# Kernel tuning notes

Measured on AMD Instinct MI355X. Metric: run time of the kernel, lower is better.

## Reference

```python
import jax, jax.numpy as jnp
import numpy as np

N_QUBITS = 6
DIM = 2 ** N_QUBITS  # 64
Q_LAYERS = 2
CHUNK = 16

# ---- single-qubit rotation gate matrices (batched over leading dim) ----

def _rx(t):
    c = jnp.cos(t / 2).astype(jnp.complex64)
    s = jnp.sin(t / 2).astype(jnp.complex64)
    return jnp.stack([jnp.stack([c, -1j * s], -1), jnp.stack([-1j * s, c], -1)], -2)

def _ry(t):
    c = jnp.cos(t / 2).astype(jnp.complex64)
    s = jnp.sin(t / 2).astype(jnp.complex64)
    return jnp.stack([jnp.stack([c, -s], -1), jnp.stack([s, c], -1)], -2)

def _rz(t):
    e = jnp.exp(-0.5j * t.astype(jnp.complex64))
    z = jnp.zeros_like(e)
    return jnp.stack([jnp.stack([e, z], -1), jnp.stack([z, jnp.conj(e)], -1)], -2)


def _apply_1q(state, gate, wire):
    # state: (B, 64) complex64; gate: (B,2,2). PennyLane wire 0 = most-significant bit.
    dl, dr = 2 ** wire, 2 ** (N_QUBITS - 1 - wire)
    s = state.reshape(-1, dl, 2, dr)
    s = jnp.einsum('bkj,bljr->blkr', gate, s)
    return s.reshape(-1, DIM)


def _apply_crx(state, theta, control, target):
    s = state.reshape((-1,) + (2,) * N_QUBITS)
    s = jnp.moveaxis(s, (control + 1, target + 1), (1, 2))
    g = _rx(theta)  # (B,2,2)
    s1 = jnp.einsum('bkj,bj...->bk...', g, s[:, 1])
    s = jnp.concatenate([s[:, :1], s1[:, None]], axis=1)
    s = jnp.moveaxis(s, (1, 2), (control + 1, target + 1))
    return s.reshape(-1, DIM)


def _ansatz(state, params, n_layers):
    # unified ansatz: per layer, RX/RY/RZ on each qubit, ring of CRX forward, ring of CRX backward
    idx = 0
    for _ in range(n_layers):
        for i in range(N_QUBITS):
            state = _apply_1q(state, _rx(params[:, idx]), i)
            state = _apply_1q(state, _ry(params[:, idx + 1]), i)
            state = _apply_1q(state, _rz(params[:, idx + 2]), i)
            idx += 3
        for i in range(N_QUBITS):
            state = _apply_crx(state, params[:, idx], i, (i + 1) % N_QUBITS)
            idx += 1
        for i in range(N_QUBITS - 1, -1, -1):
            state = _apply_crx(state, params[:, idx], i, (i - 1) % N_QUBITS)
            idx += 1
    return state


_PX = jnp.array([[0, 1], [1, 0]], jnp.complex64)
_PY = jnp.array([[0, -1j], [1j, 0]], jnp.complex64)
_PZ = jnp.array([[1, 0], [0, -1]], jnp.complex64)


def _expvals(state):
    # expectations of X_i, Y_i, Z_i for all qubits -> (B, 3*n_qubits)
    outs = []
    B = state.shape[0]
    for P in (_PX, _PY, _PZ):
        g = jnp.broadcast_to(P, (B, 2, 2))
        for i in range(N_QUBITS):
            ps = _apply_1q(state, g, i)
            outs.append(jnp.sum(jnp.conj(state) * ps, axis=1).real)
    return jnp.stack(outs, axis=1).astype(jnp.float32)


def _forward(x, emb_w, emb_b, att_w1, att_b1, att_w2, att_b2, proj_w, proj_b,
             mix_re, mix_im, qff_params, out_w, out_b, ln_g, ln_b,
             cls_w1, cls_b1, cls_w2, cls_b2):
    B, C, T = x.shape
    # classical feature extractor: (B,C,T) -> (B,T,D)
    feats = jnp.einsum('bct,cd->btd', x, emb_w) + emb_b
    D = feats.shape[-1]
    n_chunks = T // CHUNK
    xc = feats.reshape(B, n_chunks, CHUNK, D)
    # attention-weighted chunk aggregation
    h = jnp.tanh(xc @ att_w1 + att_b1)
    scores = h @ att_w2 + att_b2                      # (B,nc,CHUNK,1)
    w = jax.nn.softmax(scores, axis=2)
    chunks = jnp.sum(w * xc, axis=2)                  # (B,nc,D)
    # quantum attention core: per-chunk ansatz params
    params = jax.nn.sigmoid(chunks @ proj_w + proj_b)  # (B,nc,60)
    flat = params.reshape(B * n_chunks, -1)
    state0 = jnp.zeros((B * n_chunks, DIM), jnp.complex64).at[:, 0].set(1.0)
    evolved = _ansatz(state0, flat, Q_LAYERS).reshape(B, n_chunks, DIM)
    # LCU mixing
    coeffs = (mix_re + 1j * mix_im).astype(jnp.complex64)
    coeffs = coeffs / (jnp.abs(coeffs).sum() + 1e-8)
    mixed = jnp.einsum('bti,t->bi', evolved, coeffs)
    norms = jnp.linalg.norm(mixed, axis=1, keepdims=True)
    mixed = mixed / (norms + 1e-9)
    # quantum feed-forward (shared params) + multi-observable measurement
    qp = jnp.broadcast_to(qff_params, (B, qff_params.shape[0]))
    qstate = _ansatz(mixed, qp, 1)
    qfeat = _expvals(qstate)                          # (B,18)
    out = qfeat @ out_w + out_b                       # (B,D)
    # LayerNorm
    mu = out.mean(-1, keepdims=True)
    var = out.var(-1, keepdims=True)
    out = (out - mu) / jnp.sqrt(var + 1e-5) * ln_g + ln_b
    # classifier head
    h2 = jax.nn.relu(out @ cls_w1 + cls_b1)
    return h2 @ cls_w2 + cls_b2


def setup_inputs() -> dict:
    key = jax.random.key(0)
    ks = jax.random.split(key, 20)
    B, C, T, D = 128, 64, 2048, 256
    NC = T // CHUNK        # 128 chunks
    NCP = 5 * N_QUBITS * Q_LAYERS  # 60 circuit params
    def nrm(k, shape, scale=0.05):
        return jax.random.normal(k, shape, jnp.float32) * scale
    return {
        'x': jax.random.normal(ks[0], (B, C, T), jnp.float32),
        'emb_w': nrm(ks[1], (C, D)), 'emb_b': nrm(ks[2], (D,)),
        'att_w1': nrm(ks[3], (D, D // 2)), 'att_b1': nrm(ks[4], (D // 2,)),
        'att_w2': nrm(ks[5], (D // 2, 1)), 'att_b2': nrm(ks[6], (1,)),
        'proj_w': nrm(ks[7], (D, NCP)), 'proj_b': nrm(ks[8], (NCP,)),
        'mix_re': jax.random.uniform(ks[9], (NC,), jnp.float32),
        'mix_im': jax.random.uniform(ks[10], (NC,), jnp.float32),
        'qff_params': nrm(ks[11], (5 * N_QUBITS,), 0.1),
        'out_w': nrm(ks[12], (3 * N_QUBITS, D)), 'out_b': nrm(ks[13], (D,)),
        'ln_g': jnp.ones((D,), jnp.float32), 'ln_b': jnp.zeros((D,), jnp.float32),
        'cls_w1': nrm(ks[14], (D, D)), 'cls_b1': nrm(ks[15], (D,)),
        'cls_w2': nrm(ks[16], (D, 2)), 'cls_b2': nrm(ks[17], (2,)),
    }


def reference(x, emb_w, emb_b, att_w1, att_b1, att_w2, att_b2, proj_w, proj_b,
              mix_re, mix_im, qff_params, out_w, out_b, ln_g, ln_b,
              cls_w1, cls_b1, cls_w2, cls_b2):
    return _forward(x, emb_w, emb_b, att_w1, att_b1, att_w2, att_b2, proj_w, proj_b,
                    mix_re, mix_im, qff_params, out_w, out_b, ln_g, ln_b,
                    cls_w1, cls_b1, cls_w2, cls_b2)
```

## Files before the change

### kernel.cpp

```cpp
#include <hip/hip_runtime.h>
#include <math.h>

#define NQ    6
#define QDIM  64
#define BB    128
#define CC    64
#define TT    2048
#define DD    256
#define NCH   128
#define CHLEN 16
#define HH    128
#define NCP   60

typedef __bf16 bf16x8 __attribute__((ext_vector_type(8)));
typedef float  f32x4  __attribute__((ext_vector_type(4)));

__device__ __forceinline__ float fast_tanh(float x) {
  float e = __expf(2.f * x);
  return 1.f - 2.f / (e + 1.f);
}

__device__ __forceinline__ float wave_sum(float v) {
#pragma unroll
  for (int off = 32; off >= 1; off >>= 1) v += __shfl_xor(v, off, 64);
  return v;
}

__device__ __forceinline__ void g_rx(float& re, float& im, int lane, int m, float half) {
  float c = __cosf(half), s = __sinf(half);
  float pre = __shfl_xor(re, m, 64);
  float pim = __shfl_xor(im, m, 64);
  float nre = c * re + s * pim;
  float nim = c * im - s * pre;
  re = nre; im = nim;
}
__device__ __forceinline__ void g_ry(float& re, float& im, int lane, int m, float half) {
  float c = __cosf(half), s = __sinf(half);
  float pre = __shfl_xor(re, m, 64);
  float pim = __shfl_xor(im, m, 64);
  float sg = (lane & m) ? s : -s;
  re = c * re + sg * pre;
  im = c * im + sg * pim;
}
__device__ __forceinline__ void g_rz(float& re, float& im, int lane, int m, float half) {
  float c = __cosf(half), s = __sinf(half);
  float sg = (lane & m) ? s : -s;
  float nre = c * re - sg * im;
  float nim = c * im + sg * re;
  re = nre; im = nim;
}
__device__ __forceinline__ void g_crx(float& re, float& im, int lane, int mc, int mt, float half) {
  float c = __cosf(half), s = __sinf(half);
  float pre = __shfl_xor(re, mt, 64);
  float pim = __shfl_xor(im, mt, 64);
  if (lane & mc) {
    float nre = c * re + s * pim;
    float nim = c * im - s * pre;
    re = nre; im = nim;
  }
}
__device__ __forceinline__ void ansatz_layer(float& re, float& im, int lane,
                                             const float* p) {
#pragma unroll
  for (int q = 0; q < 6; ++q) {
    int m = 1 << (5 - q);
    g_rx(re, im, lane, m, 0.5f * p[3 * q + 0]);
    g_ry(re, im, lane, m, 0.5f * p[3 * q + 1]);
    g_rz(re, im, lane, m, 0.5f * p[3 * q + 2]);
  }
#pragma unroll
  for (int q = 0; q < 6; ++q)
    g_crx(re, im, lane, 1 << (5 - q), 1 << (5 - ((q + 1) % 6)), 0.5f * p[18 + q]);
#pragma unroll
  for (int q = 5; q >= 0; --q)
    g_crx(re, im, lane, 1 << (5 - q), 1 << (5 - ((q + 5) % 6)), 0.5f * p[24 + (5 - q)]);
}

__global__ __launch_bounds__(256) void k0_prep(
    const float* __restrict__ emb_w, const float* __restrict__ emb_b,
    const float* __restrict__ att_w1, const float* __restrict__ att_b1,
    const float* __restrict__ proj_w, const float* __restrict__ proj_b,
    __bf16* __restrict__ WfH, __bf16* __restrict__ WfL,
    __bf16* __restrict__ PfH, __bf16* __restrict__ PfL,
    float* __restrict__ b_fused, float* __restrict__ pb_fused) {
  int idx = blockIdx.x * 256 + threadIdx.x;
  if (idx < 8192) {
    int j = idx & 127, k = idx >> 7;
    float a = 0.f;
    for (int d = 0; d < 256; ++d)
      a = fmaf(emb_w[k * 256 + d], att_w1[d * 128 + j], a);
    __bf16 h = (__bf16)a;
    WfH[j * 64 + k] = h; WfL[j * 64 + k] = (__bf16)(a - (float)h);
  } else if (idx < 12288) {
    int i = idx - 8192;
    int n = i & 63, k = i >> 6;
    float a = 0.f;
    if (n < 60)
      for (int d = 0; d < 256; ++d)
        a = fmaf(emb_w[k * 256 + d], proj_w[d * 60 + n], a);
    __bf16 h = (__bf16)a;
    PfH[n * 64 + k] = h; PfL[n * 64 + k] = (__bf16)(a - (float)h);
  } else if (idx < 12416) {
    int j = idx - 12288;
    float a = att_b1[j];
    for (int d = 0; d < 256; ++d) a = fmaf(emb_b[d], att_w1[d * 128 + j], a);
    b_fused[j] = a;
  } else if (idx < 12480) {
    int n = idx - 12416;
    float a = 0.f;
    if (n < 60) {
      a = proj_b[n];
      for (int d = 0; d < 256; ++d) a = fmaf(emb_b[d], proj_w[d * 60 + n], a);
    }
    pb_fused[n] = a;
  }
}

__global__ __launch_bounds__(256) void k1_fused(
    const float* __restrict__ x, const float* __restrict__ att_w2,
    const __bf16* __restrict__ WfH, const __bf16* __restrict__ WfL,
    const __bf16* __restrict__ PfH, const __bf16* __restrict__ PfL,
    const float* __restrict__ b_fused, const float* __restrict__ pb_fused,
    float2* __restrict__ evolved) {
  const int blk = blockIdx.x;
  const int b = blk >> 6, cp = blk & 63;
  const int tid = threadIdx.x, wv = tid >> 6, lane = tid & 63;
  const int l15 = lane & 15, quad = lane >> 4;

  __shared__ float xtile[32][68];
  __shared__ float scoreS[4][32];
  __shared__ float wSm[2][16];
  __shared__ float xaggS[2][64];
  __shared__ float paramsS[2][60];

  {
#pragma unroll
    for (int pass = 0; pass < 2; ++pass) {
      int k = pass * 32 + (tid >> 3), t4 = tid & 7;
      float4 v = *(const float4*)(x + ((size_t)(b * 64 + k)) * 2048 + cp * 32 + t4 * 4);
      xtile[t4 * 4 + 0][k] = v.x; xtile[t4 * 4 + 1][k] = v.y;
      xtile[t4 * 4 + 2][k] = v.z; xtile[t4 * 4 + 3][k] = v.w;
    }
  }
  __syncthreads();

  f32x4 acc[2][2];
#pragma unroll
  for (int mt = 0; mt < 2; ++mt)
#pragma unroll
    for (int jt = 0; jt < 2; ++jt) acc[mt][jt] = (f32x4){0.f, 0.f, 0.f, 0.f};
#pragma unroll
  for (int mt = 0; mt < 2; ++mt) {
    bf16x8 ah[2], al[2];
#pragma unroll
    for (int ks = 0; ks < 2; ++ks) {
      const float* src = &xtile[mt * 16 + l15][ks * 32 + 8 * quad];
      float4 u0 = *(const float4*)src, u1 = *(const float4*)(src + 4);
      float vals[8] = {u0.x, u0.y, u0.z, u0.w, u1.x, u1.y, u1.z, u1.w};
#pragma unroll
      for (int j = 0; j < 8; ++j) {
        __bf16 h = (__bf16)vals[j];
        ah[ks][j] = h;
        al[ks][j] = (__bf16)(vals[j] - (float)h);
      }
    }
#pragma unroll
    for (int jt = 0; jt < 2; ++jt)
#pragma unroll
      for (int ks = 0; ks < 2; ++ks) {
        const size_t row = (size_t)(wv * 32 + jt * 16 + l15) * 64 + ks * 32 + 8 * quad;
        bf16x8 bh = *(const bf16x8*)(WfH + row);
        bf16x8 bl = *(const bf16x8*)(WfL + row);
        acc[mt][jt] = __builtin_amdgcn_mfma_f32_16x16x32_bf16(ah[ks], bh, acc[mt][jt], 0, 0, 0);
        acc[mt][jt] = __builtin_amdgcn_mfma_f32_16x16x32_bf16(al[ks], bh, acc[mt][jt], 0, 0, 0);
        acc[mt][jt] = __builtin_amdgcn_mfma_f32_16x16x32_bf16(ah[ks], bl, acc[mt][jt], 0, 0, 0);
      }
  }
  {
    float w2v[2], b1v[2];
#pragma unroll
    for (int jt = 0; jt < 2; ++jt) {
      int j = wv * 32 + jt * 16 + l15;
      w2v[jt] = att_w2[j];
      b1v[jt] = b_fused[j];
    }
#pragma unroll
    for (int mt = 0; mt < 2; ++mt)
#pragma unroll
      for (int r = 0; r < 4; ++r) {
        float sc = fast_tanh(acc[mt][0][r] + b1v[0]) * w2v[0] +
                   fast_tanh(acc[mt][1][r] + b1v[1]) * w2v[1];
        sc += __shfl_xor(sc, 1, 64);
        sc += __shfl_xor(sc, 2, 64);
        sc += __shfl_xor(sc, 4, 64);
        sc += __shfl_xor(sc, 8, 64);
        if (l15 == 0) scoreS[wv][mt * 16 + quad * 4 + r] = sc;
      }
  }
  __syncthreads();

  if (tid < 2) {
    float s[16], mx = -1e30f;
#pragma unroll
    for (int t = 0; t < 16; ++t) {
      int tt = tid * 16 + t;
      s[t] = (scoreS[0][tt] + scoreS[1][tt]) + (scoreS[2][tt] + scoreS[3][tt]);
      mx = fmaxf(mx, s[t]);
    }
    float sum = 0.f;
#pragma unroll
    for (int t = 0; t < 16; ++t) { s[t] = __expf(s[t] - mx); sum += s[t]; }
    float inv = 1.f / sum;
#pragma unroll
    for (int t = 0; t < 16; ++t) wSm[tid][t] = s[t] * inv;
  }
  __syncthreads();

  if (tid < 128) {
    const int c = tid >> 6, k = tid & 63;
    float a = 0.f;
#pragma unroll
    for (int t = 0; t < 16; ++t) a = fmaf(wSm[c][t], xtile[c * 16 + t][k], a);
    xaggS[c][k] = a;
  }
  __syncthreads();

  {
    const int jout = wv * 16 + l15;
    f32x4 acc3 = (f32x4){0.f, 0.f, 0.f, 0.f};
#pragma unroll
    for (int ks = 0; ks < 2; ++ks) {
      const size_t row = (size_t)jout * 64 + ks * 32 + 8 * quad;
      bf16x8 bh = *(const bf16x8*)(PfH + row);
      bf16x8 bl = *(const bf16x8*)(PfL + row);
      bf16x8 ax = (bf16x8)(__bf16)0.f, alx = (bf16x8)(__bf16)0.f;
      if (l15 < 2) {
        const float* cs = &xaggS[l15][ks * 32 + 8 * quad];
        float4 u0 = *(const float4*)cs, u1 = *(const float4*)(cs + 4);
        float vals[8] = {u0.x, u0.y, u0.z, u0.w, u1.x, u1.y, u1.z, u1.w};
#pragma unroll
        for (int j = 0; j < 8; ++j) {
          __bf16 h = (__bf16)vals[j];
          ax[j] = h;
          alx[j] = (__bf16)(vals[j] - (float)h);
        }
      }
      acc3 = __builtin_amdgcn_mfma_f32_16x16x32_bf16(ax, bh, acc3, 0, 0, 0);
      acc3 = __builtin_amdgcn_mfma_f32_16x16x32_bf16(alx, bh, acc3, 0, 0, 0);
      acc3 = __builtin_amdgcn_mfma_f32_16x16x32_bf16(ax, bl, acc3, 0, 0, 0);
    }
    if (jout < 60 && quad == 0) {
      float pbias = pb_fused[jout];
#pragma unroll
      for (int r = 0; r < 2; ++r) {
        float a = acc3[r] + pbias;
        paramsS[r][jout] = 1.f / (1.f + __expf(-a));
      }
    }
  }
  __syncthreads();

  if (wv < 2) {
    float re = (lane == 0) ? 1.f : 0.f, im = 0.f;
    const float* p = paramsS[wv];
    ansatz_layer(re, im, lane, p);
    ansatz_layer(re, im, lane, p + 30);
    evolved[((size_t)b * NCH + cp * 2 + wv) * QDIM + lane] = make_float2(re, im);
  }
}

__global__ __launch_bounds__(512) void k3_head(
    const float2* __restrict__ evolved, const float* __restrict__ mix_re,
    const float* __restrict__ mix_im, const float* __restrict__ qff,
    const float* __restrict__ out_w, const float* __restrict__ out_b,
    const float* __restrict__ ln_g, const float* __restrict__ ln_b,
    const float* __restrict__ cls_w1, const float* __restrict__ cls_b1,
    const float* __restrict__ cls_w2, const float* __restrict__ cls_b2,
    float* __restrict__ outp) {
  const int b = blockIdx.x, tid = threadIdx.x, wv = tid >> 6, lane = tid & 63;
  __shared__ float mreS[8][64], mimS[8][64];
  __shared__ float qfeatS[18];
  __shared__ float outS[DD];
  __shared__ float redS[8];
  __shared__ float clsR[2][DD];

  float are = 0.f, aim = 0.f;
#pragma unroll 4
  for (int t = wv * 16; t < wv * 16 + 16; ++t) {
    float2 e = evolved[((size_t)b * NCH + t) * QDIM + lane];
    float cr = mix_re[t], ci = mix_im[t];
    are = fmaf(cr, e.x, are); are = fmaf(-ci, e.y, are);
    aim = fmaf(cr, e.y, aim); aim = fmaf(ci, e.x, aim);
  }
  mreS[wv][lane] = are; mimS[wv][lane] = aim;
  __syncthreads();

  if (wv == 0) {
    float r0 = mix_re[lane], i0 = mix_im[lane];
    float r1 = mix_re[lane + 64], i1 = mix_im[lane + 64];
    float sp = sqrtf(r0 * r0 + i0 * i0) + sqrtf(r1 * r1 + i1 * i1);
    float S = wave_sum(sp) + 1e-8f;
    float re = 0.f, im = 0.f;
#pragma unroll
    for (int w = 0; w < 8; ++w) { re += mreS[w][lane]; im += mimS[w][lane]; }
    float invS = 1.f / S;
    re *= invS; im *= invS;
    float n2 = wave_sum(re * re + im * im);
    float scl = 1.f / (sqrtf(n2) + 1e-9f);
    re *= scl; im *= scl;
    float qp[30];
#pragma unroll
    for (int i = 0; i < 30; ++i) qp[i] = qff[i];
    ansatz_layer(re, im, lane, qp);
#pragma unroll
    for (int q = 0; q < 6; ++q) {
      int m = 1 << (5 - q);
      float pre = __shfl_xor(re, m, 64), pim = __shfl_xor(im, m, 64);
      float vx = re * pre + im * pim;
      float vy = (lane & m) ? (im * pre - re * pim) : (re * pim - im * pre);
      float vz = (lane & m) ? -(re * re + im * im) : (re * re + im * im);
      vx = wave_sum(vx); vy = wave_sum(vy); vz = wave_sum(vz);
      if (lane == 0) { qfeatS[q] = vx; qfeatS[6 + q] = vy; qfeatS[12 + q] = vz; }
    }
  }
  __syncthreads();

  float o = 0.f, dv = 0.f;
  if (tid < 256) {
    o = out_b[tid];
#pragma unroll
    for (int k = 0; k < 18; ++k) o = fmaf(qfeatS[k], out_w[k * DD + tid], o);
    float s1 = wave_sum(o);
    if (lane == 0) redS[wv] = s1;
  }
  __syncthreads();
  float mu = (redS[0] + redS[1] + redS[2] + redS[3]) * (1.f / 256.f);
  if (tid < 256) {
    dv = o - mu;
    float s2 = wave_sum(dv * dv);
    if (lane == 0) redS[wv] = s2;
  }
  __syncthreads();
  float var = (redS[0] + redS[1] + redS[2] + redS[3]) * (1.f / 256.f);
  if (tid < 256) {
    outS[tid] = dv / sqrtf(var + 1e-5f) * ln_g[tid] + ln_b[tid];
  }
  __syncthreads();

  {
    const int dd = tid & 255, hh = tid >> 8;
    float r = (hh == 0) ? cls_b1[dd] : 0.f;
#pragma unroll 8
    for (int d = hh * 128; d < hh * 128 + 128; ++d)
      r = fmaf(outS[d], cls_w1[(size_t)d * DD + dd], r);
    clsR[hh][dd] = r;
  }
  __syncthreads();
  if (tid < 256) {
    float r = fmaxf(clsR[0][tid] + clsR[1][tid], 0.f);
    float p0 = wave_sum(r * cls_w2[tid * 2 + 0]);
    float p1 = wave_sum(r * cls_w2[tid * 2 + 1]);
    if (lane == 0) { mreS[0][wv] = p0; mreS[1][wv] = p1; }
  }
  __syncthreads();
  if (tid == 0) {
    outp[b * 2 + 0] = (mreS[0][0] + mreS[0][1]) + (mreS[0][2] + mreS[0][3]) + cls_b2[0];
    outp[b * 2 + 1] = (mreS[1][0] + mreS[1][1]) + (mreS[1][2] + mreS[1][3]) + cls_b2[1];
  }
}

extern "C" void kernel_launch(void* const* d_in, const int* in_sizes, int n_in,
                              void* d_out, int out_size, void* d_ws, size_t ws_size,
                              hipStream_t stream) {
  const float* x      = (const float*)d_in[0];
  const float* emb_w  = (const float*)d_in[1];
  const float* emb_b  = (const float*)d_in[2];
  const float* att_w1 = (const float*)d_in[3];
  const float* att_b1 = (const float*)d_in[4];
  const float* att_w2 = (const float*)d_in[5];
  const float* proj_w = (const float*)d_in[7];
  const float* proj_b = (const float*)d_in[8];
  const float* mix_re = (const float*)d_in[9];
  const float* mix_im = (const float*)d_in[10];
  const float* qff    = (const float*)d_in[11];
  const float* out_w  = (const float*)d_in[12];
  const float* out_b  = (const float*)d_in[13];
  const float* ln_g   = (const float*)d_in[14];
  const float* ln_b   = (const float*)d_in[15];
  const float* cls_w1 = (const float*)d_in[16];
  const float* cls_b1 = (const float*)d_in[17];
  const float* cls_w2 = (const float*)d_in[18];
  const float* cls_b2 = (const float*)d_in[19];

  char* ws = (char*)d_ws;
  float2* evolved = (float2*)ws;
  size_t off = 8388608;
  __bf16* WfH = (__bf16*)(ws + off); off += 16384;
  __bf16* WfL = (__bf16*)(ws + off); off += 16384;
  __bf16* PfH = (__bf16*)(ws + off); off += 8192;
  __bf16* PfL = (__bf16*)(ws + off); off += 8192;
  float* b_fused  = (float*)(ws + off); off += 512;
  float* pb_fused = (float*)(ws + off); off += 256;

  k0_prep<<<49, 256, 0, stream>>>(emb_w, emb_b, att_w1, att_b1, proj_w, proj_b,
                                  WfH, WfL, PfH, PfL, b_fused, pb_fused);
  k1_fused<<<BB * 64, 256, 0, stream>>>(
      x, att_w2, WfH, WfL, PfH, PfL, b_fused, pb_fused, evolved);
  k3_head<<<BB, 512, 0, stream>>>(evolved, mix_re, mix_im, qff, out_w, out_b,
                                  ln_g, ln_b, cls_w1, cls_b1, cls_w2, cls_b2,
                                  (float*)d_out);
}
```

Before: 217.4 us.

## Precompute fused rotation matrices and split-bf16 operands in shared memory

Converts the x tile into hi/lo bf16 fragments once per block in shared memory instead of once per wave, and stores the aggregated vector already split. The softmax is spread across 32 lanes with shuffles instead of two serial threads. RX·RY·RZ per qubit is precomputed into one 2x2 complex matrix, and CRX cos/sin values are tabulated, so the state-vector simulation applies one shuffle-based gate per qubit. The cost is extra syncthreads and a shared-memory union whose aliasing must be correct.

After: 211.0 us. 1.03x faster.

```diff
diff --git a/kernel.cpp b/kernel.cpp
--- a/kernel.cpp
+++ b/kernel.cpp
@@ -129,9 +129,16 @@
 
   __shared__ float xtile[32][68];
   __shared__ float scoreS[4][32];
-  __shared__ float wSm[2][16];
-  __shared__ float xaggS[2][64];
-  __shared__ float paramsS[2][60];
+  __shared__ float4 uniF4[512];
+  char* uni = (char*)uniF4;
+  bf16x8* afH = (bf16x8*)uni;
+  bf16x8* afL = (bf16x8*)(uni + 4096);
+  float*  wSm     = (float*)uni;
+  __bf16* axH     = (__bf16*)(uni + 128);
+  __bf16* axL     = (__bf16*)(uni + 384);
+  float*  paramsS = (float*)(uni + 640);
+  float4* matS    = (float4*)(uni + 1120);
+  float2* crxS    = (float2*)(uni + 1888);
 
   {
 #pragma unroll
@@ -144,6 +151,23 @@
   }
   __syncthreads();
 
+  {
+    const int mt = tid >> 7, ks = (tid >> 6) & 1, ln = tid & 63;
+    const float* src = &xtile[mt * 16 + (ln & 15)][ks * 32 + (ln >> 4) * 8];
+    float4 u0 = *(const float4*)src, u1 = *(const float4*)(src + 4);
+    float vals[8] = {u0.x, u0.y, u0.z, u0.w, u1.x, u1.y, u1.z, u1.w};
+    bf16x8 h, l;
+#pragma unroll
+    for (int j = 0; j < 8; ++j) {
+      __bf16 hh = (__bf16)vals[j];
+      h[j] = hh;
+      l[j] = (__bf16)(vals[j] - (float)hh);
+    }
+    afH[(mt * 2 + ks) * 64 + ln] = h;
+    afL[(mt * 2 + ks) * 64 + ln] = l;
+  }
+  __syncthreads();
+
   f32x4 acc[2][2];
 #pragma unroll
   for (int mt = 0; mt < 2; ++mt)
@@ -154,15 +178,8 @@
     bf16x8 ah[2], al[2];
 #pragma unroll
     for (int ks = 0; ks < 2; ++ks) {
-      const float* src = &xtile[mt * 16 + l15][ks * 32 + 8 * quad];
-      float4 u0 = *(const float4*)src, u1 = *(const float4*)(src + 4);
-      float vals[8] = {u0.x, u0.y, u0.z, u0.w, u1.x, u1.y, u1.z, u1.w};
-#pragma unroll
-      for (int j = 0; j < 8; ++j) {
-        __bf16 h = (__bf16)vals[j];
-        ah[ks][j] = h;
-        al[ks][j] = (__bf16)(vals[j] - (float)h);
-      }
+      ah[ks] = afH[(mt * 2 + ks) * 64 + lane];
+      al[ks] = afL[(mt * 2 + ks) * 64 + lane];
     }
 #pragma unroll
     for (int jt = 0; jt < 2; ++jt)
@@ -199,20 +216,21 @@
   }
   __syncthreads();
 
-  if (tid < 2) {
-    float s[16], mx = -1e30f;
-#pragma unroll
-    for (int t = 0; t < 16; ++t) {
-      int tt = tid * 16 + t;
-      s[t] = (scoreS[0][tt] + scoreS[1][tt]) + (scoreS[2][tt] + scoreS[3][tt]);
-      mx = fmaxf(mx, s[t]);
-    }
-    float sum = 0.f;
-#pragma unroll
-    for (int t = 0; t < 16; ++t) { s[t] = __expf(s[t] - mx); sum += s[t]; }
-    float inv = 1.f / sum;
-#pragma unroll
-    for (int t = 0; t < 16; ++t) wSm[tid][t] = s[t] * inv;
+  if (tid < 32) {
+    const int c = tid >> 4, t = tid & 15, ct = c * 16 + t;
+    float s = (scoreS[0][ct] + scoreS[1][ct]) + (scoreS[2][ct] + scoreS[3][ct]);
+    float mx = s;
+    mx = fmaxf(mx, __shfl_xor(mx, 1, 64));
+    mx = fmaxf(mx, __shfl_xor(mx, 2, 64));
+    mx = fmaxf(mx, __shfl_xor(mx, 4, 64));
+    mx = fmaxf(mx, __shfl_xor(mx, 8, 64));
+    float e = __expf(s - mx);
+    float sum = e;
+    sum += __shfl_xor(sum, 1, 64);
+    sum += __shfl_xor(sum, 2, 64);
+    sum += __shfl_xor(sum, 4, 64);
+    sum += __shfl_xor(sum, 8, 64);
+    wSm[ct] = e / sum;
   }
   __syncthreads();
 
@@ -220,8 +238,10 @@
     const int c = tid >> 6, k = tid & 63;
     float a = 0.f;
 #pragma unroll
-    for (int t = 0; t < 16; ++t) a = fmaf(wSm[c][t], xtile[c * 16 + t][k], a);
-    xaggS[c][k] = a;
+    for (int t = 0; t < 16; ++t) a = fmaf(wSm[c * 16 + t], xtile[c * 16 + t][k], a);
+    __bf16 h = (__bf16)a;
+    axH[c * 64 + k] = h;
+    axL[c * 64 + k] = (__bf16)(a - (float)h);
   }
   __syncthreads();
 
@@ -235,15 +255,8 @@
       bf16x8 bl = *(const bf16x8*)(PfL + row);
       bf16x8 ax = (bf16x8)(__bf16)0.f, alx = (bf16x8)(__bf16)0.f;
       if (l15 < 2) {
-        const float* cs = &xaggS[l15][ks * 32 + 8 * quad];
-        float4 u0 = *(const float4*)cs, u1 = *(const float4*)(cs + 4);
-        float vals[8] = {u0.x, u0.y, u0.z, u0.w, u1.x, u1.y, u1.z, u1.w};
-#pragma unroll
-        for (int j = 0; j < 8; ++j) {
-          __bf16 h = (__bf16)vals[j];
-          ax[j] = h;
-          alx[j] = (__bf16)(vals[j] - (float)h);
-        }
+        ax  = *(const bf16x8*)(axH + l15 * 64 + ks * 32 + 8 * quad);
+        alx = *(const bf16x8*)(axL + l15 * 64 + ks * 32 + 8 * quad);
       }
       acc3 = __builtin_amdgcn_mfma_f32_16x16x32_bf16(ax, bh, acc3, 0, 0, 0);
       acc3 = __builtin_amdgcn_mfma_f32_16x16x32_bf16(alx, bh, acc3, 0, 0, 0);
@@ -251,20 +264,76 @@
     }
     if (jout < 60 && quad == 0) {
       float pbias = pb_fused[jout];
+      const int layer = (jout >= 30) ? 1 : 0;
+      const int pm = jout - layer * 30;
 #pragma unroll
       for (int r = 0; r < 2; ++r) {
         float a = acc3[r] + pbias;
-        paramsS[r][jout] = 1.f / (1.f + __expf(-a));
-      }
-    }
+        float p = 1.f / (1.f + __expf(-a));
+        paramsS[r * 60 + jout] = p;
+        if (pm >= 18) {
+          float sn, cs;
+          __sincosf(0.5f * p, &sn, &cs);
+          crxS[r * 24 + layer * 12 + (pm - 18)] = make_float2(cs, sn);
+        }
+      }
+    }
+  }
+  __syncthreads();
+
+  if (tid < 24) {
+    const int r = tid / 12, g = tid % 12;
+    const float* pp = paramsS + r * 60 + (g / 6) * 30 + (g % 6) * 3;
+    float sa, ca, sb, cb, sg, cg;
+    __sincosf(0.5f * pp[0], &sa, &ca);
+    __sincosf(0.5f * pp[1], &sb, &cb);
+    __sincosf(0.5f * pp[2], &sg, &cg);
+    float m00r = cb * ca, m00i = sb * sa;
+    float m01r = -sb * ca, m01i = -cb * sa;
+    float m10r = sb * ca, m10i = -cb * sa;
+    float m11r = cb * ca, m11i = -sb * sa;
+    float4 b0, b1;
+    b0.x = cg * m00r + sg * m00i;  b0.y = cg * m00i - sg * m00r;
+    b0.z = cg * m01r + sg * m01i;  b0.w = cg * m01i - sg * m01r;
+    b1.x = cg * m11r - sg * m11i;  b1.y = cg * m11i + sg * m11r;
+    b1.z = cg * m10r - sg * m10i;  b1.w = cg * m10i + sg * m10r;
+    matS[(r * 12 + g) * 2 + 0] = b0;
+    matS[(r * 12 + g) * 2 + 1] = b1;
   }
   __syncthreads();
 
   if (wv < 2) {
     float re = (lane == 0) ? 1.f : 0.f, im = 0.f;
-    const float* p = paramsS[wv];
-    ansatz_layer(re, im, lane, p);
-    ansatz_layer(re, im, lane, p + 30);
+    const float4* mats = matS + wv * 24;
+    const float2* crxs = crxS + wv * 24;
+#pragma unroll
+    for (int l = 0; l < 2; ++l) {
+#pragma unroll
+      for (int q = 0; q < 6; ++q) {
+        const int m = 1 << (5 - q);
+        float4 M = mats[(l * 6 + q) * 2 + ((lane & m) ? 1 : 0)];
+        float pre = __shfl_xor(re, m, 64);
+        float pim = __shfl_xor(im, m, 64);
+        float nre = M.x * re - M.y * im + M.z * pre - M.w * pim;
+        float nim = M.x * im + M.y * re + M.z * pim + M.w * pre;
+        re = nre; im = nim;
+      }
+#pragma unroll
+      for (int e = 0; e < 12; ++e) {
+        const int q = (e < 6) ? e : (11 - e);
+        const int mc = 1 << (5 - q);
+        const int mt = (e < 6) ? (1 << (5 - ((q + 1) % 6)))
+                               : (1 << (5 - ((q + 5) % 6)));
+        float2 cs = crxs[l * 12 + e];
+        float pre = __shfl_xor(re, mt, 64);
+        float pim = __shfl_xor(im, mt, 64);
+        float nre = fmaf(cs.y, pim, cs.x * re);
+        float nim = fmaf(-cs.y, pre, cs.x * im);
+        bool act = (lane & mc) != 0;
+        re = act ? nre : re;
+        im = act ? nim : im;
+      }
+    }
     evolved[((size_t)b * NCH + cp * 2 + wv) * QDIM + lane] = make_float2(re, im);
   }
 }
```
